# Performance work log

Hardware: AMD Instinct MI355X
Metric: run time of the kernel (lower is better)

Reference implementation:

```python
import jax, jax.numpy as jnp
import numpy as np

N = 20000      # nodes
E = 400000     # edges
D = 256        # input_dim == hidden_dim
L = 4          # num_layers
EIN = 32       # edgenet_input_dim // 2
EH = 128       # edge parser hidden
NC = 2         # num_classes
JK = L * D     # 1024
BN_EPS = 1e-5


def setup_inputs() -> dict:
    key = jax.random.key(0)
    ks = jax.random.split(key, 16)
    s = 0.05
    inp = {
        "features": jax.random.normal(ks[0], (N, D), jnp.float32),
        "edge_index": jax.random.randint(ks[1], (2, E), 0, N, dtype=jnp.int64),
        "edgenet_input": jax.random.normal(ks[2], (E, 2 * EIN), jnp.float32),
        # ChebConv weights: [layer, k, in, out] (all layers 256->256, K=3, no bias)
        "cheb_w": jax.random.normal(ks[3], (L, 3, D, D), jnp.float32) * s,
        # EdgeEncoder (PAE-style) parser: Linear(32,128)+ReLU+BN+Linear(128,128)
        "en_w1": jax.random.normal(ks[4], (EIN, EH), jnp.float32) * s,
        "en_b1": jnp.zeros((EH,), jnp.float32),
        "en_g1": jnp.ones((EH,), jnp.float32),
        "en_be1": jnp.zeros((EH,), jnp.float32),
        "en_w2": jax.random.normal(ks[5], (EH, EH), jnp.float32) * s,
        "en_b2": jnp.zeros((EH,), jnp.float32),
        # cls head: Linear(1024,256)+ReLU+BN(256)+Linear(256,2)
        "cls_w1": jax.random.normal(ks[6], (JK, 256), jnp.float32) * s,
        "cls_b1": jnp.zeros((256,), jnp.float32),
        "cls_g": jnp.ones((256,), jnp.float32),
        "cls_b": jnp.zeros((256,), jnp.float32),
        "cls_w2": jax.random.normal(ks[7], (256, NC), jnp.float32) * s,
        "cls_b2": jnp.zeros((NC,), jnp.float32),
    }
    return inp


def _bn_eval(x, g, b):
    # eval-mode BatchNorm1d with fresh running stats (mean=0, var=1)
    return x * (g / jnp.sqrt(1.0 + BN_EPS)) + b


def reference(features, edge_index, edgenet_input, cheb_w,
              en_w1, en_b1, en_g1, en_be1, en_w2, en_b2,
              cls_w1, cls_b1, cls_g, cls_b, cls_w2, cls_b2):
    row, col = edge_index[0], edge_index[1]

    # ---- EdgeEncoder (PAE): shared parser on both halves + cosine sim ----
    def parser(x):
        h = jnp.maximum(x @ en_w1 + en_b1, 0.0)
        h = _bn_eval(h, en_g1, en_be1)
        return h @ en_w2 + en_b2

    half = edgenet_input.shape[1] // 2
    h1 = parser(edgenet_input[:, :half])
    h2 = parser(edgenet_input[:, half:])
    n1 = jnp.maximum(jnp.linalg.norm(h1, axis=1), 1e-8)
    n2 = jnp.maximum(jnp.linalg.norm(h2, axis=1), 1e-8)
    cos = jnp.sum(h1 * h2, axis=1) / (n1 * n2)
    edge_weight = (cos + 1.0) * 0.5  # [E]

    # ---- ChebConv sym normalization (lambda_max=2): L_hat = -D^-1/2 A D^-1/2 ----
    deg = jax.ops.segment_sum(edge_weight, row, num_segments=N)
    dis = jnp.where(deg > 0, jax.lax.rsqrt(jnp.maximum(deg, 1e-30)), 0.0)
    norm = -dis[row] * edge_weight * dis[col]  # [E]

    def prop(x):  # out[col] += norm * x[row]
        return jax.ops.segment_sum(x[row] * norm[:, None], col, num_segments=N)

    # ---- stacked ChebConv (K=3, no bias) + ReLU + JK concat ----
    x = features
    jk = None
    for i in range(L):
        W = cheb_w[i]
        Tx0 = x
        Tx1 = prop(Tx0)
        Tx2 = 2.0 * prop(Tx1) - Tx0
        h = jnp.maximum(Tx0 @ W[0] + Tx1 @ W[1] + Tx2 @ W[2], 0.0)
        jk = h if i == 0 else jnp.concatenate([jk, h], axis=1)
        x = h

    # ---- cls head ----
    z = jnp.maximum(jk @ cls_w1 + cls_b1, 0.0)
    z = _bn_eval(z, cls_g, cls_b)
    logit = z @ cls_w2 + cls_b2
    return (logit, edge_weight)
```

## Files before the change

### kernel.cpp

```cpp
#include <hip/hip_runtime.h>
#include <hip/hip_bf16.h>

#define NN 20000
#define EE 400000
#define RSBN 0.9999950000374997f

typedef __attribute__((ext_vector_type(8))) short short8;
typedef __attribute__((ext_vector_type(8))) unsigned short ushort8;
typedef __attribute__((ext_vector_type(4))) short bf4;
typedef __attribute__((ext_vector_type(4))) float floatx4;

__device__ __forceinline__ short f2bf(float f) {
  union { float f; unsigned u; } v; v.f = f;
  unsigned r = v.u + 0x7fffu + ((v.u >> 16) & 1u);
  return (short)(r >> 16);
}
__device__ __forceinline__ unsigned f2bf2(float x, float y) {
  union { __hip_bfloat162 h; unsigned u; } v;
  v.h = __float22bfloat162_rn(make_float2(x, y));
  return v.u;
}
__device__ __forceinline__ float bf2f(unsigned short u) {
  union { unsigned u; float f; } v; v.u = ((unsigned)u) << 16;
  return v.f;
}
__device__ __forceinline__ void gl_lds16(const void* g, void* l) {
  __builtin_amdgcn_global_load_lds(
      (const __attribute__((address_space(1))) unsigned*)g,
      (__attribute__((address_space(3))) unsigned*)l, 16, 0, 0);
}

__device__ __forceinline__ floatx4 mfma16(bf4 a, bf4 b, floatx4 c) {
#if __has_builtin(__builtin_amdgcn_mfma_f32_16x16x16bf16_1k)
  return __builtin_amdgcn_mfma_f32_16x16x16bf16_1k(a, b, c, 0, 0, 0);
#else
  floatx4 d;
  asm volatile("v_mfma_f32_16x16x16_bf16 %0, %1, %2, %3"
               : "=&v"(d) : "v"(a), "v"(b), "v"(c));
  return d;
#endif
}

__device__ __forceinline__ float dpp_xor1(float x) {
  union { float f; int i; } a, b;
  a.f = x;
  b.i = __builtin_amdgcn_update_dpp(0, a.i, 0xB1, 0xF, 0xF, false);
  return b.f;
}

__device__ __forceinline__ int xcd_swizzle(int bid, int nwg) {
  int q = nwg >> 3, r = nwg & 7;
  int x = bid & 7, o = bid >> 3;
  return (x < r ? x * (q + 1) : r * (q + 1) + (x - r) * q) + o;
}

__global__ __launch_bounds__(256) void ewconv_kernel(
    const float* __restrict__ w1, const float* __restrict__ w2,
    const float* __restrict__ g1, const float* __restrict__ be1,
    const float* __restrict__ b1, const float* __restrict__ b2,
    unsigned short* __restrict__ ewf)
{
  int tid = threadIdx.x;
#pragma unroll
  for (int i = 0; i < 16; i++) {
    int idx = i * 256 + tid;
    int k = idx >> 7, n = idx & 127;
    int pos = ((n >> 4) * 64 + (k >> 3) * 16 + (n & 15)) * 8 + (k & 7);
    ewf[pos] = f2bf(w1[idx]);
  }
#pragma unroll
  for (int i = 0; i < 64; i++) {
    int idx = i * 256 + tid;
    int k = idx >> 7, n = idx & 127;
    int u = k >> 4, q = (k >> 2) & 3, j = k & 3;
    int t = n >> 4, l = n & 15;
    int pos = (((u * 8 + t) * 4 + q) * 16 + l) * 4 + j;
    ewf[4096 + pos] = f2bf(w2[idx] * g1[k] * RSBN);
  }
  float* fb = (float*)(ewf + 20480);
  if (tid < 128) {
    fb[tid] = b1[tid];
    float acc = b2[tid];
    for (int k = 0; k < 128; k++) acc += be1[k] * w2[k * 128 + tid] * g1[k] * RSBN;
    fb[128 + tid] = acc;
  }
}

__global__ __launch_bounds__(512, 4) void edge_kernel(
    const float* __restrict__ xin, const int* __restrict__ eidx,
    const unsigned short* __restrict__ ewf,
    float* __restrict__ ew_out,
    float* __restrict__ deg, int* __restrict__ cnt)
{
  __shared__ short wbuf[20992];

  int tid = threadIdx.x;
  int lane = tid & 63;
  int wv = tid >> 6;
  int l15 = lane & 15;
  int quad = lane >> 4;

#pragma unroll
  for (int i = 0; i < 5; i++)
    gl_lds16(ewf + (i * 512 + tid) * 8, &wbuf[(i * 512 + tid) * 8]);
  if (tid < 64)
    gl_lds16(ewf + (2560 + tid) * 8, &wbuf[(2560 + tid) * 8]);

  const short* w1f = wbuf;
  const short* w2f = wbuf + 4096;

  int rowA = blockIdx.x * 256 + wv * 16;
  int rowB = rowA + 128;

  short8 afA, afB;
  {
    const float* xpA = xin + (size_t)(rowA + l15) * 32 + quad * 8;
    const float* xpB = xin + (size_t)(rowB + l15) * 32 + quad * 8;
    float4 a0 = *(const float4*)xpA;
    float4 a1 = *(const float4*)(xpA + 4);
    float4 b0 = *(const float4*)xpB;
    float4 b1v = *(const float4*)(xpB + 4);
    union { short8 s; unsigned u[4]; } a, b;
    a.u[0] = f2bf2(a0.x, a0.y); a.u[1] = f2bf2(a0.z, a0.w);
    a.u[2] = f2bf2(a1.x, a1.y); a.u[3] = f2bf2(a1.z, a1.w);
    b.u[0] = f2bf2(b0.x, b0.y); b.u[1] = f2bf2(b0.z, b0.w);
    b.u[2] = f2bf2(b1v.x, b1v.y); b.u[3] = f2bf2(b1v.z, b1v.w);
    afA = a.s; afB = b.s;
  }

  __syncthreads();

  const float* fb = (const float*)(wbuf + 20480);

  floatx4 acc1A[8], acc1B[8];
#pragma unroll
  for (int t = 0; t < 8; t++) {
    floatx4 z = *(const floatx4*)&fb[t * 16 + quad * 4];
    short8 w1v = *(const short8*)&w1f[(t * 64 + lane) * 8];
    acc1A[t] = __builtin_amdgcn_mfma_f32_16x16x32_bf16(w1v, afA, z, 0, 0, 0);
    acc1B[t] = __builtin_amdgcn_mfma_f32_16x16x32_bf16(w1v, afB, z, 0, 0, 0);
  }

  bf4 pbA[8], pbB[8];
#pragma unroll
  for (int u = 0; u < 8; u++) {
    union { bf4 s; unsigned w[2]; } oa, ob;
    oa.w[0] = f2bf2(fmaxf(acc1A[u][0], 0.f), fmaxf(acc1A[u][1], 0.f));
    oa.w[1] = f2bf2(fmaxf(acc1A[u][2], 0.f), fmaxf(acc1A[u][3], 0.f));
    ob.w[0] = f2bf2(fmaxf(acc1B[u][0], 0.f), fmaxf(acc1B[u][1], 0.f));
    ob.w[1] = f2bf2(fmaxf(acc1B[u][2], 0.f), fmaxf(acc1B[u][3], 0.f));
    pbA[u] = oa.s; pbB[u] = ob.s;
  }

  floatx4 acc2A[8], acc2B[8];
#pragma unroll
  for (int t = 0; t < 8; t++) {
    floatx4 z2 = *(const floatx4*)&fb[128 + t * 16 + quad * 4];
    acc2A[t] = z2; acc2B[t] = z2;
  }
#pragma unroll
  for (int u = 0; u < 8; u++)
#pragma unroll
    for (int t = 0; t < 8; t++) {
      bf4 a4 = *(const bf4*)&w2f[((u * 8 + t) * 64 + lane) * 4];
      acc2A[t] = mfma16(a4, pbA[u], acc2A[t]);
      acc2B[t] = mfma16(a4, pbB[u], acc2B[t]);
    }

#pragma unroll
  for (int tile = 0; tile < 2; tile++) {
    floatx4* acc2 = tile ? acc2B : acc2A;
    int rowbase = tile ? rowB : rowA;
    float qq = 0.f, pp = 0.f;
#pragma unroll
    for (int t = 0; t < 8; t++)
#pragma unroll
      for (int r = 0; r < 4; r++) {
        float h = acc2[t][r];
        float hp = dpp_xor1(h);
        qq += h * h;
        pp += h * hp;
      }
    qq += __shfl_xor(qq, 16, 64);
    pp += __shfl_xor(pp, 16, 64);
    qq += __shfl_xor(qq, 32, 64);
    pp += __shfl_xor(pp, 32, 64);
    float rr = dpp_xor1(qq);

    if (quad == 0 && !(l15 & 1)) {
      int e = (rowbase + l15) >> 1;
      float n1 = fmaxf(sqrtf(qq), 1e-8f);
      float n2 = fmaxf(sqrtf(rr), 1e-8f);
      float w = (pp / (n1 * n2) + 1.f) * 0.5f;
      ew_out[e] = w;
      atomicAdd(deg + eidx[e], w);
      atomicAdd(cnt + eidx[EE + e], 1);
    }
  }
}

__global__ __launch_bounds__(256) void fconv_kernel(const float* __restrict__ src,
                                                    unsigned short* __restrict__ dst) {
  size_t i = ((size_t)blockIdx.x * 256 + threadIdx.x) * 8;
  float4 a = *(const float4*)(src + i);
  float4 b = *(const float4*)(src + i + 4);
  union { ushort8 s; unsigned u[4]; } o;
  o.u[0] = f2bf2(a.x, a.y); o.u[1] = f2bf2(a.z, a.w);
  o.u[2] = f2bf2(b.x, b.y); o.u[3] = f2bf2(b.z, b.w);
  *(ushort8*)(dst + i) = o.s;
}

__global__ __launch_bounds__(256) void wconv_kernel(
    const float* __restrict__ cheb_w, const float* __restrict__ cls_w1,
    unsigned short* __restrict__ wtc, unsigned short* __restrict__ clsT)
{
  __shared__ unsigned short tile[64][80];
  int z = blockIdx.z;
  const float* src; const float* src2 = nullptr; float scale = 1.f;
  unsigned short* dst; int ldk;
  if (z < 12) {
    int l = z / 3, c = z % 3;
    src = cheb_w + (size_t)z * 65536;
    if (c == 0) src2 = cheb_w + (size_t)(l * 3 + 2) * 65536;
    if (c == 2) scale = 2.f;
    dst = wtc + (size_t)l * 196608 + c * 256;
    ldk = 768;
  } else {
    int c = z - 12;
    src = cls_w1 + (size_t)c * 65536;
    dst = clsT + c * 256;
    ldk = 1024;
  }
  int t = threadIdx.x;
  int k0 = blockIdx.x * 64, n0 = blockIdx.y * 64;
#pragma unroll
  for (int pass = 0; pass < 4; pass++) {
    int kk = pass * 16 + (t >> 4);
    int nl = (t & 15) * 4;
    size_t offe = (size_t)(k0 + kk) * 256 + n0 + nl;
    float4 v = *(const float4*)(src + offe);
    if (src2) {
      float4 v2 = *(const float4*)(src2 + offe);
      v.x -= v2.x; v.y -= v2.y; v.z -= v2.z; v.w -= v2.w;
    } else if (scale != 1.f) {
      v.x *= scale; v.y *= scale; v.z *= scale; v.w *= scale;
    }
    tile[nl + 0][kk] = f2bf(v.x);
    tile[nl + 1][kk] = f2bf(v.y);
    tile[nl + 2][kk] = f2bf(v.z);
    tile[nl + 3][kk] = f2bf(v.w);
  }
  __syncthreads();
  int nl = t >> 2, kc = (t & 3) * 16;
  ushort8 v0 = *(const ushort8*)&tile[nl][kc];
  ushort8 v1 = *(const ushort8*)&tile[nl][kc + 8];
  unsigned short* dp = dst + (size_t)(n0 + nl) * ldk + k0 + kc;
  *(ushort8*)dp = v0;
  *(ushort8*)(dp + 8) = v1;
}

__global__ __launch_bounds__(1024) void scan_kernel(const int* __restrict__ cnt, int* __restrict__ ptr) {
  __shared__ int sums[1024];
  int tid = threadIdx.x;
  const int n = NN;
  const int chunk = (n + 1023) / 1024;
  int base = tid * chunk;
  int s = 0;
  for (int i = 0; i < chunk; i++) {
    int idx = base + i;
    if (idx < n) s += (cnt[idx] + 3) & ~3;
  }
  sums[tid] = s;
  __syncthreads();
  for (int off = 1; off < 1024; off <<= 1) {
    int v = (tid >= off) ? sums[tid - off] : 0;
    __syncthreads();
    sums[tid] += v;
    __syncthreads();
  }
  int run = (tid == 0) ? 0 : sums[tid - 1];
  for (int i = 0; i < chunk; i++) {
    int idx = base + i;
    if (idx < n) { ptr[idx] = run; run += (cnt[idx] + 3) & ~3; }
  }
  if (tid == 1023) ptr[n] = run;
}

__global__ __launch_bounds__(256) void hist_kernel(const int* __restrict__ cnt,
                                                   int* __restrict__ hist) {
  __shared__ int lh[64];
  int tid = threadIdx.x;
  if (tid < 64) lh[tid] = 0;
  __syncthreads();
  int i = blockIdx.x * 256 + tid;
  if (i < NN) {
    int b = (cnt[i] + 3) >> 2; if (b > 63) b = 63;
    atomicAdd(&lh[b], 1);
  }
  __syncthreads();
  if (tid < 64 && lh[tid]) atomicAdd(&hist[tid], lh[tid]);
}

__global__ void binscan_kernel(const int* __restrict__ hist,
                               int* __restrict__ binbase, int* __restrict__ binfill) {
  int tid = threadIdx.x;
  int v = hist[tid];
  int x = v;
#pragma unroll
  for (int off = 1; off < 64; off <<= 1) {
    int y = __shfl_up(x, off, 64);
    if (tid >= off) x += y;
  }
  binbase[tid] = x - v;
  binfill[tid] = 0;
}

__global__ __launch_bounds__(256) void perm_kernel(const int* __restrict__ cnt,
                                                   const int* __restrict__ binbase,
                                                   int* __restrict__ binfill,
                                                   int* __restrict__ perm) {
  __shared__ int lh[64], lbase[64];
  int tid = threadIdx.x;
  if (tid < 64) lh[tid] = 0;
  __syncthreads();
  int i = blockIdx.x * 256 + tid;
  int b = 0, local = 0;
  bool valid = (i < NN);
  if (valid) {
    b = (cnt[i] + 3) >> 2; if (b > 63) b = 63;
    local = atomicAdd(&lh[b], 1);
  }
  __syncthreads();
  if (tid < 64 && lh[tid]) lbase[tid] = atomicAdd(&binfill[tid], lh[tid]);
  __syncthreads();
  if (valid) perm[binbase[b] + lbase[b] + local] = i;
}

__global__ void fill_kernel(const int* __restrict__ eidx, const float* __restrict__ ew,
                            const float* __restrict__ deg, const int* __restrict__ ptr,
                            int* __restrict__ fill, unsigned short* __restrict__ cidx,
                            float* __restrict__ cval) {
  int e = blockIdx.x * 256 + threadIdx.x;
  if (e < EE) {
    int r = eidx[e], c = eidx[EE + e];
    float dr = deg[r], dc = deg[c];
    float ir = dr > 0.f ? 1.f / sqrtf(fmaxf(dr, 1e-30f)) : 0.f;
    float ic = dc > 0.f ? 1.f / sqrtf(fmaxf(dc, 1e-30f)) : 0.f;
    float nv = -ir * ew[e] * ic;
    int pos = ptr[c] + atomicAdd(&fill[c], 1);
    cidx[pos] = (unsigned short)r;
    cval[pos] = nv;
  }
}

__global__ __launch_bounds__(256) void prop_kernel(
    const unsigned short* __restrict__ x, int ldx,
    const unsigned short* __restrict__ cidx, const float* __restrict__ cval,
    const int* __restrict__ ptr, const int* __restrict__ perm,
    unsigned short* __restrict__ y, int ldy)
{
  int sliceid = blockIdx.x & 7;
  int colslice = sliceid >> 1;
  int chunk = (blockIdx.x >> 3) * 2 + (sliceid & 1);
  int ci = chunk * 32 + (threadIdx.x >> 3);
  if (ci >= NN) return;
  int c = perm[ci];
  int d = colslice * 64 + (threadIdx.x & 7) * 8;
  int p0 = ptr[c], p1 = ptr[c + 1];
  float a[8] = {0.f, 0.f, 0.f, 0.f, 0.f, 0.f, 0.f, 0.f};

#define PLOAD(P, R, W, V0, V1, V2, V3)                                  \
  do {                                                                  \
    R = *(const ushort4*)(cidx + (P));                                  \
    W = *(const float4*)(cval + (P));                                   \
    V0 = *(const ushort8*)(x + (size_t)R.x * ldx + d);                  \
    V1 = *(const ushort8*)(x + (size_t)R.y * ldx + d);                  \
    V2 = *(const ushort8*)(x + (size_t)R.z * ldx + d);                  \
    V3 = *(const ushort8*)(x + (size_t)R.w * ldx + d);                  \
  } while (0)

#define PACC(W, V0, V1, V2, V3)                                         \
  do {                                                                  \
    _Pragma("unroll")                                                   \
    for (int j = 0; j < 8; j++)                                         \
      a[j] += W.x * bf2f(V0[j]) + W.y * bf2f(V1[j]) +                   \
              W.z * bf2f(V2[j]) + W.w * bf2f(V3[j]);                    \
  } while (0)

  if (p0 < p1) {
    int n4 = (p1 - p0) >> 2;
    ushort4 rA, rB; float4 wA, wB;
    ushort8 vA0, vA1, vA2, vA3, vB0, vB1, vB2, vB3;
    PLOAD(p0, rA, wA, vA0, vA1, vA2, vA3);
    if (n4 == 1) {
      PACC(wA, vA0, vA1, vA2, vA3);
    } else {
      PLOAD(p0 + 4, rB, wB, vB0, vB1, vB2, vB3);
      int p = p0 + 8;
      if (n4 & 1) {
        PACC(wA, vA0, vA1, vA2, vA3);
        PLOAD(p, rA, wA, vA0, vA1, vA2, vA3);
        p += 4;
      }
      for (; p < p1; p += 8) {
        PACC(wA, vA0, vA1, vA2, vA3);
        PLOAD(p, rA, wA, vA0, vA1, vA2, vA3);
        PACC(wB, vB0, vB1, vB2, vB3);
        PLOAD(p + 4, rB, wB, vB0, vB1, vB2, vB3);
      }
      PACC(wA, vA0, vA1, vA2, vA3);
      PACC(wB, vB0, vB1, vB2, vB3);
    }
  }
#undef PLOAD
#undef PACC

  union { ushort8 s; unsigned u[4]; } o;
#pragma unroll
  for (int j = 0; j < 8; j += 2)
    o.u[j >> 1] = f2bf2(a[j], a[j + 1]);
  *(ushort8*)(y + (size_t)c * ldy + d) = o.s;
}

__global__ __launch_bounds__(256, 4) void mgemm_kernel(
    const unsigned short* A0, const unsigned short* A1,
    const unsigned short* A2, const unsigned short* A3,
    int l0, int l1, int l2, int l3, int nchunks,
    const unsigned short* __restrict__ BT, int ldbt,
    unsigned short* __restrict__ Cb, float* __restrict__ Cf, int ldc, int M,
    const float* __restrict__ bias, const float* __restrict__ bng,
    const float* __restrict__ bnb)
{
  __shared__ short As[4 * 64 * 8];
  __shared__ short Bs[4 * 128 * 8];
  int tid = threadIdx.x;
  int lane = tid & 63;
  int wv = tid >> 6;
  int l15 = lane & 15, quad = lane >> 4;
  int wr = wv >> 1, wc = wv & 1;
  int bidx = xcd_swizzle(blockIdx.x, gridDim.x);
  int m0 = bidx * 64, n0 = blockIdx.y * 128;

  const unsigned short* Ap[4] = {A0, A1, A2, A3};
  int Al[4] = {l0, l1, l2, l3};

  int arow = tid & 63, ac = tid >> 6;
  int brow = tid & 127, bc = tid >> 7;

  floatx4 acc[2][4];
#pragma unroll
  for (int mi = 0; mi < 2; mi++)
#pragma unroll
    for (int nj = 0; nj < 4; nj++) acc[mi][nj] = (floatx4){0.f, 0.f, 0.f, 0.f};

  for (int c = 0; c < nchunks; c++) {
    const unsigned short* Abase = Ap[c] + (size_t)(m0 + arow) * Al[c] + ac * 8;
    const unsigned short* Bbase = BT + (size_t)(n0 + brow) * ldbt + c * 256 + bc * 8;
#pragma unroll 1
    for (int kb = 0; kb < 256; kb += 32) {
      __syncthreads();
      gl_lds16(Abase + kb, &As[tid * 8]);
      gl_lds16(Bbase + kb, &Bs[tid * 8]);
      gl_lds16(Bbase + 16 + kb, &Bs[(tid + 256) * 8]);
      __syncthreads();
      short8 af[2], bfv[4];
#pragma unroll
      for (int mi = 0; mi < 2; mi++)
        af[mi] = *(const short8*)&As[(quad * 64 + wr * 32 + mi * 16 + l15) * 8];
#pragma unroll
      for (int nj = 0; nj < 4; nj++)
        bfv[nj] = *(const short8*)&Bs[(quad * 128 + wc * 64 + nj * 16 + l15) * 8];
#pragma unroll
      for (int nj = 0; nj < 4; nj++)
#pragma unroll
        for (int mi = 0; mi < 2; mi++)
          acc[mi][nj] = __builtin_amdgcn_mfma_f32_16x16x32_bf16(af[mi], bfv[nj], acc[mi][nj], 0, 0, 0);
    }
  }

  if (Cb) {
#pragma unroll
    for (int mi = 0; mi < 2; mi++)
#pragma unroll
      for (int r = 0; r < 4; r++) {
        int row = m0 + wr * 32 + mi * 16 + quad * 4 + r;
        if (row < M) {
#pragma unroll
          for (int nj = 0; nj < 4; nj++) {
            int col = n0 + wc * 64 + nj * 16 + l15;
            Cb[(size_t)row * ldc + col] = (unsigned short)f2bf(fmaxf(acc[mi][nj][r], 0.f));
          }
        }
      }
  } else {
    float bs[4], g[4], bb[4];
#pragma unroll
    for (int nj = 0; nj < 4; nj++) {
      int col = n0 + wc * 64 + nj * 16 + l15;
      bs[nj] = bias[col]; g[nj] = bng[col] * RSBN; bb[nj] = bnb[col];
    }
#pragma unroll
    for (int mi = 0; mi < 2; mi++)
#pragma unroll
      for (int r = 0; r < 4; r++) {
        int row = m0 + wr * 32 + mi * 16 + quad * 4 + r;
        if (row < M) {
#pragma unroll
          for (int nj = 0; nj < 4; nj++) {
            int col = n0 + wc * 64 + nj * 16 + l15;
            float v = fmaxf(acc[mi][nj][r] + bs[nj], 0.f) * g[nj] + bb[nj];
            Cf[(size_t)row * ldc + col] = v;
          }
        }
      }
  }
}

__global__ __launch_bounds__(256) void logit_kernel(
    const float* __restrict__ z, const float* __restrict__ w2,
    const float* __restrict__ b2, float* __restrict__ out)
{
  int node = blockIdx.x * 4 + (threadIdx.x >> 6);
  if (node >= NN) return;
  int lane = threadIdx.x & 63;
  int k = lane * 4;
  float4 zv = *(const float4*)(z + (size_t)node * 256 + k);
  float4 wa = *(const float4*)(w2 + k * 2);
  float4 wb = *(const float4*)(w2 + k * 2 + 4);
  float a0 = zv.x * wa.x + zv.y * wa.z + zv.z * wb.x + zv.w * wb.z;
  float a1 = zv.x * wa.y + zv.y * wa.w + zv.z * wb.y + zv.w * wb.w;
#pragma unroll
  for (int m = 32; m >= 1; m >>= 1) {
    a0 += __shfl_xor(a0, m, 64);
    a1 += __shfl_xor(a1, m, 64);
  }
  if (lane == 0) {
    out[(size_t)node * 2]     = a0 + b2[0];
    out[(size_t)node * 2 + 1] = a1 + b2[1];
  }
}

extern "C" void kernel_launch(void* const* d_in, const int* in_sizes, int n_in,
                              void* d_out, int out_size, void* d_ws, size_t ws_size,
                              hipStream_t stream) {
  const float* features = (const float*)d_in[0];
  const int*   eidx     = (const int*)d_in[1];
  const float* xin      = (const float*)d_in[2];
  const float* cheb_w   = (const float*)d_in[3];
  const float* en_w1    = (const float*)d_in[4];
  const float* en_b1    = (const float*)d_in[5];
  const float* en_g1    = (const float*)d_in[6];
  const float* en_be1   = (const float*)d_in[7];
  const float* en_w2    = (const float*)d_in[8];
  const float* en_b2    = (const float*)d_in[9];
  const float* cls_w1   = (const float*)d_in[10];
  const float* cls_b1   = (const float*)d_in[11];
  const float* cls_g    = (const float*)d_in[12];
  const float* cls_b    = (const float*)d_in[13];
  const float* cls_w2   = (const float*)d_in[14];
  const float* cls_b2   = (const float*)d_in[15];
  float* out = (float*)d_out;

  char* ws = (char*)d_ws;
  size_t off = 0;
  auto alloc = [&](size_t bytes) -> void* {
    void* p = ws + off;
    off += (bytes + 255) & ~(size_t)255;
    return p;
  };
  const int CSRN = EE + 4 * NN;
  float* deg  = (float*)alloc((size_t)NN * 4);
  int*   cnt  = (int*)  alloc((size_t)NN * 4);
  int*   fil  = (int*)  alloc((size_t)NN * 4);
  int*   hist = (int*)  alloc(64 * 4);
  float* cval = (float*)alloc((size_t)CSRN * 4);
  unsigned short* cidx = (unsigned short*)alloc((size_t)CSRN * 2);
  size_t zero_len = off;
  int*   ptr  = (int*)  alloc((size_t)(NN + 1) * 4);
  int*   perm = (int*)  alloc((size_t)NN * 4);
  int*   binbase = (int*)alloc(64 * 4);
  int*   binfill = (int*)alloc(64 * 4);
  unsigned short* featb = (unsigned short*)alloc((size_t)NN * 256 * 2);
  unsigned short* Tx1   = (unsigned short*)alloc((size_t)NN * 256 * 2);
  unsigned short* Tx2   = (unsigned short*)alloc((size_t)NN * 256 * 2);
  unsigned short* jk    = (unsigned short*)alloc((size_t)NN * 1024 * 2);
  float* zbuf = (float*)alloc((size_t)NN * 256 * 4);
  unsigned short* wtc   = (unsigned short*)alloc((size_t)4 * 196608 * 2);
  unsigned short* clsT  = (unsigned short*)alloc((size_t)256 * 1024 * 2);
  unsigned short* ewf   = (unsigned short*)alloc((size_t)20992 * 2);
  alloc(262144);

  float* ew = out + (size_t)NN * 2;

  hipMemsetAsync(deg, 0, zero_len, stream);

  ewconv_kernel<<<1, 256, 0, stream>>>(en_w1, en_w2, en_g1, en_be1, en_b1, en_b2, ewf);
  edge_kernel<<<3125, 512, 0, stream>>>(xin, eidx, ewf, ew, deg, cnt);
  fconv_kernel<<<2500, 256, 0, stream>>>(features, featb);
  wconv_kernel<<<dim3(4, 4, 16), 256, 0, stream>>>(cheb_w, cls_w1, wtc, clsT);
  scan_kernel<<<1, 1024, 0, stream>>>(cnt, ptr);
  hist_kernel<<<(NN + 255) / 256, 256, 0, stream>>>(cnt, hist);
  binscan_kernel<<<1, 64, 0, stream>>>(hist, binbase, binfill);
  perm_kernel<<<(NN + 255) / 256, 256, 0, stream>>>(cnt, binbase, binfill, perm);
  fill_kernel<<<(EE + 255) / 256, 256, 0, stream>>>(eidx, ew, deg, ptr, fil, cidx, cval);

  dim3 ggrid(313, 2);
  for (int i = 0; i < 4; i++) {
    const unsigned short* x = (i == 0) ? featb : (jk + (size_t)(i - 1) * 256);
    int ldx = (i == 0) ? 256 : 1024;
    prop_kernel<<<2504, 256, 0, stream>>>(x, ldx, cidx, cval, ptr, perm, Tx1, 256);
    prop_kernel<<<2504, 256, 0, stream>>>(Tx1, 256, cidx, cval, ptr, perm, Tx2, 256);
    mgemm_kernel<<<ggrid, 256, 0, stream>>>(x, Tx1, Tx2, nullptr, ldx, 256, 256, 0, 3,
                                            wtc + (size_t)i * 196608, 768,
                                            jk + (size_t)i * 256, nullptr, 1024, NN,
                                            nullptr, nullptr, nullptr);
  }

  mgemm_kernel<<<ggrid, 256, 0, stream>>>(jk, jk + 256, jk + 512, jk + 768,
                                          1024, 1024, 1024, 1024, 4, clsT, 1024,
                                          nullptr, zbuf, 256, NN,
                                          cls_b1, cls_g, cls_b);
  logit_kernel<<<NN / 4, 256, 0, stream>>>(zbuf, cls_w2, cls_b2, out);
}
```

Before: 638.4 us.

## Pack CSR row index and bf16 weight into one word; remap prop threads

The CSR column index (16-bit) and the normalized edge weight, now rounded to bf16, are packed into a single 32-bit word, so each prop step issues one uint4 load instead of separate index and value loads, and the CSR footprint shrinks. The prop kernel's thread mapping also changes: 4 threads per node over 32-column slices, 64 nodes per block and 8 column slices, in place of 8 threads over 64 columns. The edge weights lose precision from fp32 to bf16, and the narrower per-node slices raise the number of index reads per node across blocks.

```diff
diff --git a/kernel.cpp b/kernel.cpp
--- a/kernel.cpp
+++ b/kernel.cpp
@@ -338,8 +338,7 @@
 
 __global__ void fill_kernel(const int* __restrict__ eidx, const float* __restrict__ ew,
                             const float* __restrict__ deg, const int* __restrict__ ptr,
-                            int* __restrict__ fill, unsigned short* __restrict__ cidx,
-                            float* __restrict__ cval) {
+                            int* __restrict__ fill, unsigned* __restrict__ epack) {
   int e = blockIdx.x * 256 + threadIdx.x;
   if (e < EE) {
     int r = eidx[e], c = eidx[EE + e];
@@ -348,68 +347,69 @@
     float ic = dc > 0.f ? 1.f / sqrtf(fmaxf(dc, 1e-30f)) : 0.f;
     float nv = -ir * ew[e] * ic;
     int pos = ptr[c] + atomicAdd(&fill[c], 1);
-    cidx[pos] = (unsigned short)r;
-    cval[pos] = nv;
+    epack[pos] = ((unsigned)r << 16) | (unsigned short)f2bf(nv);
   }
 }
 
 __global__ __launch_bounds__(256) void prop_kernel(
     const unsigned short* __restrict__ x, int ldx,
-    const unsigned short* __restrict__ cidx, const float* __restrict__ cval,
+    const unsigned* __restrict__ epack,
     const int* __restrict__ ptr, const int* __restrict__ perm,
     unsigned short* __restrict__ y, int ldy)
 {
-  int sliceid = blockIdx.x & 7;
-  int colslice = sliceid >> 1;
-  int chunk = (blockIdx.x >> 3) * 2 + (sliceid & 1);
-  int ci = chunk * 32 + (threadIdx.x >> 3);
+  int colslice = blockIdx.x & 7;
+  int chunk = blockIdx.x >> 3;
+  int ci = chunk * 64 + (threadIdx.x >> 2);
   if (ci >= NN) return;
   int c = perm[ci];
-  int d = colslice * 64 + (threadIdx.x & 7) * 8;
+  int d = colslice * 32 + (threadIdx.x & 3) * 8;
   int p0 = ptr[c], p1 = ptr[c + 1];
   float a[8] = {0.f, 0.f, 0.f, 0.f, 0.f, 0.f, 0.f, 0.f};
 
-#define PLOAD(P, R, W, V0, V1, V2, V3)                                  \
+#define PLOAD(P, PK, V0, V1, V2, V3)                                    \
   do {                                                                  \
-    R = *(const ushort4*)(cidx + (P));                                  \
-    W = *(const float4*)(cval + (P));                                   \
-    V0 = *(const ushort8*)(x + (size_t)R.x * ldx + d);                  \
-    V1 = *(const ushort8*)(x + (size_t)R.y * ldx + d);                  \
-    V2 = *(const ushort8*)(x + (size_t)R.z * ldx + d);                  \
-    V3 = *(const ushort8*)(x + (size_t)R.w * ldx + d);                  \
+    PK = *(const uint4*)(epack + (P));                                  \
+    V0 = *(const ushort8*)(x + (size_t)(PK.x >> 16) * ldx + d);         \
+    V1 = *(const ushort8*)(x + (size_t)(PK.y >> 16) * ldx + d);         \
+    V2 = *(const ushort8*)(x + (size_t)(PK.z >> 16) * ldx + d);         \
+    V3 = *(const ushort8*)(x + (size_t)(PK.w >> 16) * ldx + d);         \
   } while (0)
 
-#define PACC(W, V0, V1, V2, V3)                                         \
+#define PACC(PK, V0, V1, V2, V3)                                        \
   do {                                                                  \
+    float w0 = bf2f((unsigned short)(PK.x & 0xffffu));                  \
+    float w1 = bf2f((unsigned short)(PK.y & 0xffffu));                  \
+    float w2 = bf2f((unsigned short)(PK.z & 0xffffu));                  \
+    float w3 = bf2f((unsigned short)(PK.w & 0xffffu));                  \
     _Pragma("unroll")                                                   \
     for (int j = 0; j < 8; j++)                                         \
-      a[j] += W.x * bf2f(V0[j]) + W.y * bf2f(V1[j]) +                   \
-              W.z * bf2f(V2[j]) + W.w * bf2f(V3[j]);                    \
+      a[j] += w0 * bf2f(V0[j]) + w1 * bf2f(V1[j]) +                     \
+              w2 * bf2f(V2[j]) + w3 * bf2f(V3[j]);                      \
   } while (0)
 
   if (p0 < p1) {
     int n4 = (p1 - p0) >> 2;
-    ushort4 rA, rB; float4 wA, wB;
+    uint4 kA, kB;
     ushort8 vA0, vA1, vA2, vA3, vB0, vB1, vB2, vB3;
-    PLOAD(p0, rA, wA, vA0, vA1, vA2, vA3);
+    PLOAD(p0, kA, vA0, vA1, vA2, vA3);
     if (n4 == 1) {
-      PACC(wA, vA0, vA1, vA2, vA3);
+      PACC(kA, vA0, vA1, vA2, vA3);
     } else {
-      PLOAD(p0 + 4, rB, wB, vB0, vB1, vB2, vB3);
+      PLOAD(p0 + 4, kB, vB0, vB1, vB2, vB3);
       int p = p0 + 8;
       if (n4 & 1) {
-        PACC(wA, vA0, vA1, vA2, vA3);
-        PLOAD(p, rA, wA, vA0, vA1, vA2, vA3);
+        PACC(kA, vA0, vA1, vA2, vA3);
+        PLOAD(p, kA, vA0, vA1, vA2, vA3);
         p += 4;
       }
       for (; p < p1; p += 8) {
-        PACC(wA, vA0, vA1, vA2, vA3);
-        PLOAD(p, rA, wA, vA0, vA1, vA2, vA3);
-        PACC(wB, vB0, vB1, vB2, vB3);
-        PLOAD(p + 4, rB, wB, vB0, vB1, vB2, vB3);
+        PACC(kA, vA0, vA1, vA2, vA3);
+        PLOAD(p, kA, vA0, vA1, vA2, vA3);
+        PACC(kB, vB0, vB1, vB2, vB3);
+        PLOAD(p + 4, kB, vB0, vB1, vB2, vB3);
       }
-      PACC(wA, vA0, vA1, vA2, vA3);
-      PACC(wB, vB0, vB1, vB2, vB3);
+      PACC(kA, vA0, vA1, vA2, vA3);
+      PACC(kB, vB0, vB1, vB2, vB3);
     }
   }
 #undef PLOAD
@@ -573,8 +573,7 @@
   int*   cnt  = (int*)  alloc((size_t)NN * 4);
   int*   fil  = (int*)  alloc((size_t)NN * 4);
   int*   hist = (int*)  alloc(64 * 4);
-  float* cval = (float*)alloc((size_t)CSRN * 4);
-  unsigned short* cidx = (unsigned short*)alloc((size_t)CSRN * 2);
+  unsigned* epack = (unsigned*)alloc((size_t)CSRN * 4);
   size_t zero_len = off;
   int*   ptr  = (int*)  alloc((size_t)(NN + 1) * 4);
   int*   perm = (int*)  alloc((size_t)NN * 4);
@@ -602,14 +601,14 @@
   hist_kernel<<<(NN + 255) / 256, 256, 0, stream>>>(cnt, hist);
   binscan_kernel<<<1, 64, 0, stream>>>(hist, binbase, binfill);
   perm_kernel<<<(NN + 255) / 256, 256, 0, stream>>>(cnt, binbase, binfill, perm);
-  fill_kernel<<<(EE + 255) / 256, 256, 0, stream>>>(eidx, ew, deg, ptr, fil, cidx, cval);
+  fill_kernel<<<(EE + 255) / 256, 256, 0, stream>>>(eidx, ew, deg, ptr, fil, epack);
 
   dim3 ggrid(313, 2);
   for (int i = 0; i < 4; i++) {
     const unsigned short* x = (i == 0) ? featb : (jk + (size_t)(i - 1) * 256);
     int ldx = (i == 0) ? 256 : 1024;
-    prop_kernel<<<2504, 256, 0, stream>>>(x, ldx, cidx, cval, ptr, perm, Tx1, 256);
-    prop_kernel<<<2504, 256, 0, stream>>>(Tx1, 256, cidx, cval, ptr, perm, Tx2, 256);
+    prop_kernel<<<313 * 8, 256, 0, stream>>>(x, ldx, epack, ptr, perm, Tx1, 256);
+    prop_kernel<<<313 * 8, 256, 0, stream>>>(Tx1, 256, epack, ptr, perm, Tx2, 256);
     mgemm_kernel<<<ggrid, 256, 0, stream>>>(x, Tx1, Tx2, nullptr, ldx, 256, 256, 0, 3,
                                             wtc + (size_t)i * 196608, 768,
                                             jk + (size_t)i * 256, nullptr, 1024, NN,
```

Result: slower. 690.1 us (+8.1%).
